# Optimization experiments

Measured on AMD Instinct MI355X. Metric: run time of the kernel, lower is better.

The kernel has to match this reference:

```python
import jax, jax.numpy as jnp
import numpy as np

IN_FEATURES = 4096
OUT_FEATURES = 11008
BATCH, SEQ = 4, 2048


def setup_inputs() -> dict:
    key = jax.random.key(0)
    k_x, k_w, k_b = jax.random.split(key, 3)
    x = jax.random.normal(k_x, (BATCH, SEQ, IN_FEATURES), dtype=jnp.float32)
    # int8-valued quantized weight (stored int32 for portability; values in [-127,127])
    weight_int8 = jax.random.randint(k_w, (OUT_FEATURES, IN_FEATURES), -127, 128, dtype=jnp.int32)
    # per-tensor symmetric quantization scale (max|w|/127 in original; any positive scalar)
    scale = jnp.float32(0.01)
    bias = jax.random.normal(k_b, (OUT_FEATURES,), dtype=jnp.float32) * 0.02
    return {"x": x, "weight_int8": weight_int8, "scale": scale, "bias": bias}


def reference(x, weight_int8, scale, bias):
    # Codec is lossless: decompress() yields the int8 tensor exactly, then
    # dequantizes: w = int8.astype(float) * scale; forward is F.linear(x, w, bias).
    w = weight_int8.astype(jnp.float32) * scale  # [out, in]
    # x: [b, s, in] @ w.T -> [b, s, out]
    return jnp.einsum("bsi,oi->bso", x, w) + bias
```

## Files before the change

kernel.cpp:

```cpp
#include <hip/hip_runtime.h>
#include <stdint.h>


#define M_DIM 8192
#define N_DIM 11008
#define K_DIM 4096

#define BM 256
#define BN 256
#define BK 32
#define NT (K_DIM / BK)
#define NBN (N_DIM / BN)
#define NBM (M_DIM / BM)
#define GRID (NBM * NBN)

typedef short bf16x8 __attribute__((ext_vector_type(8)));
typedef float f32x4 __attribute__((ext_vector_type(4)));
typedef float fvec4 __attribute__((ext_vector_type(4)));
typedef int   ivec4 __attribute__((ext_vector_type(4)));
typedef unsigned short usvec4 __attribute__((ext_vector_type(4)));

__device__ __forceinline__ unsigned short f2bf(float f) {
    union { float f; uint32_t u; } c; c.f = f;
    uint32_t u = c.u;
    return (unsigned short)((u + 0x7FFFu + ((u >> 16) & 1u)) >> 16);
}

__global__ __launch_bounds__(256) void cvt_fused_kernel(
    const float* __restrict__ x, const int* __restrict__ w,
    unsigned short* __restrict__ xo, unsigned short* __restrict__ wo)
{
    const int NX4 = M_DIM * K_DIM / 4;
    const int NW4 = N_DIM * K_DIM / 4;
    const int stride = gridDim.x * blockDim.x;
    const int t0 = blockIdx.x * blockDim.x + threadIdx.x;
    for (int i = t0; i < NX4; i += stride) {
        fvec4 v = __builtin_nontemporal_load(&((const fvec4*)x)[i]);
        usvec4 r;
        r.x = f2bf(v.x); r.y = f2bf(v.y); r.z = f2bf(v.z); r.w = f2bf(v.w);
        ((usvec4*)xo)[i] = r;
    }
    for (int i = t0; i < NW4; i += stride) {
        ivec4 v = __builtin_nontemporal_load(&((const ivec4*)w)[i]);
        usvec4 r;
        r.x = f2bf((float)v.x); r.y = f2bf((float)v.y);
        r.z = f2bf((float)v.z); r.w = f2bf((float)v.w);
        ((usvec4*)wo)[i] = r;
    }
}

__device__ __forceinline__ void async16(const void* g, void* l) {
    __builtin_amdgcn_global_load_lds((__attribute__((address_space(1))) void*)g,
                                     (__attribute__((address_space(3))) void*)l,
                                     16, 0, 0);
}


__global__ __launch_bounds__(512, 2) void gemm_bf16_kernel(
    const unsigned short* __restrict__ A,
    const unsigned short* __restrict__ B,
    const float* __restrict__ scale_p,
    const float* __restrict__ bias,
    float* __restrict__ out)
{
    __shared__ __attribute__((aligned(16))) char lds[131072];

    const int t    = threadIdx.x;
    const int lane = t & 63;
    const int w    = t >> 6;
    const int wm   = w >> 2;
    const int wn   = w & 3;
    const int quad = lane >> 4;
    const int l16  = lane & 15;

    const int bid = blockIdx.x;
    const int swz = (bid & 7) * (GRID / 8) + (bid >> 3);
    const int bm = swz / NBN;
    const int bn = swz % NBN;

    f32x4 acc[8][4];
#pragma unroll
    for (int i = 0; i < 8; i++)
#pragma unroll
        for (int j = 0; j < 4; j++)
            acc[i][j] = (f32x4){0.f, 0.f, 0.f, 0.f};

    const int rowh = t >> 2;
    const int slot = t & 3;
    const int csw  = ((slot ^ ((rowh >> 1) & 3)) << 4);
    const char* aS0 = (const char*)(A + (size_t)(bm * BM + rowh) * K_DIM) + csw;
    const char* bS0 = (const char*)(B + (size_t)(bn * BN + rowh) * K_DIM) + csw;
    const char* aS1 = aS0 + (size_t)128 * K_DIM * 2;
    const char* bS1 = bS0 + (size_t)128 * K_DIM * 2;
    char* aD = lds + t * 16;
    char* bD = lds + 65536 + t * 16;

#define STAGE(buf, kt) do { \
        const size_t kb_ = (size_t)(kt) * (BK * 2); \
        async16(aS0 + kb_, aD + ((buf) << 14)); \
        async16(aS1 + kb_, aD + ((buf) << 14) + 8192); \
        async16(bS0 + kb_, bD + ((buf) << 14)); \
        async16(bS1 + kb_, bD + ((buf) << 14) + 8192); \
    } while (0)

    const int coff = ((quad ^ ((l16 >> 1) & 3)) << 4);
    const int aoff = (wm * 128 + l16) * (BK * 2) + coff;
    const int boff = 65536 + (wn * 64 + l16) * (BK * 2) + coff;

    bf16x8 fa[8], fb[4], ga[8], gb[4];

    STAGE(0, 0); STAGE(1, 1); STAGE(2, 2);
    asm volatile("s_waitcnt vmcnt(8)" ::: "memory");
    __builtin_amdgcn_s_barrier();
    asm volatile("" ::: "memory");
#pragma unroll
    for (int j = 0; j < 4; j++) fb[j] = *(const bf16x8*)(lds + boff + j * 1024);
#pragma unroll
    for (int i = 0; i < 8; i++) fa[i] = *(const bf16x8*)(lds + aoff + i * 1024);

    auto body = [&](int kt, bf16x8 (&ca)[8], bf16x8 (&cb)[4],
                    bf16x8 (&na)[8], bf16x8 (&nb)[4]) __attribute__((always_inline)) {
        STAGE((kt + 3) & 3, (kt + 3) & (NT - 1));
        asm volatile("s_waitcnt vmcnt(8)" ::: "memory");
        __builtin_amdgcn_s_barrier();
        asm volatile("" ::: "memory");

        const char* Abn = lds + (((kt + 1) & 3) << 14) + aoff;
        const char* Bbn = lds + (((kt + 1) & 3) << 14) + boff;
#pragma unroll
        for (int j = 0; j < 4; j++) nb[j] = *(const bf16x8*)(Bbn + j * 1024);
#pragma unroll
        for (int i = 0; i < 8; i++) na[i] = *(const bf16x8*)(Abn + i * 1024);

        __builtin_amdgcn_s_setprio(1);
#pragma unroll
        for (int i = 0; i < 8; i++)
#pragma unroll
            for (int j = 0; j < 4; j++)
                acc[i][j] = __builtin_amdgcn_mfma_f32_16x16x32_bf16(
                    ca[i], cb[j], acc[i][j], 0, 0, 0);
        __builtin_amdgcn_s_setprio(0);
    };

    for (int kt = 0; kt < NT; kt += 2) {
        body(kt,     fa, fb, ga, gb);
        body(kt + 1, ga, gb, fa, fb);
    }
#undef STAGE

    const float scale = *scale_p;
    const int gcol = bn * BN + wn * 64 + l16;
    float bvals[4];
#pragma unroll
    for (int j = 0; j < 4; j++) bvals[j] = bias[gcol + j * 16];

#pragma unroll
    for (int i = 0; i < 8; i++) {
        const int grow0 = bm * BM + wm * 128 + i * 16 + quad * 4;
#pragma unroll
        for (int r = 0; r < 4; r++) {
            float* orow = out + (size_t)(grow0 + r) * N_DIM + gcol;
#pragma unroll
            for (int j = 0; j < 4; j++)
                orow[j * 16] = acc[i][j][r] * scale + bvals[j];
        }
    }
}

__global__ __launch_bounds__(256) void naive_kernel(
    const float* __restrict__ x, const int* __restrict__ w8,
    const float* __restrict__ scale_p, const float* __restrict__ bias,
    float* __restrict__ out)
{
    size_t idx = (size_t)blockIdx.x * 256 + threadIdx.x;
    if (idx >= (size_t)M_DIM * N_DIM) return;
    int n = (int)(idx % N_DIM);
    size_t m = idx / N_DIM;
    const float* xr = x + m * K_DIM;
    const int* wr = w8 + (size_t)n * K_DIM;
    float acc = 0.f;
    for (int k = 0; k < K_DIM; k++) acc += xr[k] * (float)wr[k];
    out[idx] = acc * (*scale_p) + bias[n];
}

extern "C" void kernel_launch(void* const* d_in, const int* in_sizes, int n_in,
                              void* d_out, int out_size, void* d_ws, size_t ws_size,
                              hipStream_t stream) {
    const float* x     = (const float*)d_in[0];
    const int*   w8    = (const int*)d_in[1];
    const float* scale = (const float*)d_in[2];
    const float* bias  = (const float*)d_in[3];
    float* out = (float*)d_out;

    const size_t a_bytes = (size_t)M_DIM * K_DIM * 2;
    const size_t b_bytes = (size_t)N_DIM * K_DIM * 2;

    if (ws_size >= a_bytes + b_bytes) {
        unsigned short* a_bf = (unsigned short*)d_ws;
        unsigned short* b_bf = (unsigned short*)((char*)d_ws + a_bytes);
        cvt_fused_kernel<<<2048, 256, 0, stream>>>(x, w8, a_bf, b_bf);
        gemm_bf16_kernel<<<GRID, 512, 0, stream>>>(a_bf, b_bf, scale, bias, out);
    } else {
        size_t total = (size_t)M_DIM * N_DIM;
        naive_kernel<<<(unsigned)((total + 255) / 256), 256, 0, stream>>>(
            x, w8, scale, bias, out);
    }
}
```

Baseline: 1.182 ms.

## Make bf16 GEMM persistent with cross-tile prefetch and nontemporal stores

Converts the GEMM into a persistent kernel with 256 blocks. Each block walks a strided set of tiles within its XCD chunk and prefetches the next tile's first K stages while finishing the current one. The barrier now comes before issuing the next async stage, with a tighter vmcnt wait. Output stores use nontemporal hints, and the conversion kernel launches more blocks. This aims to remove per-tile prologue bubbles and launch tail costs. In exchange, the wave tail becomes coarse (5 vs 6 tiles per block) and the code is more complex.

```diff
diff --git a/kernel.cpp b/kernel.cpp
--- a/kernel.cpp
+++ b/kernel.cpp
@@ -13,6 +13,8 @@
 #define NBN (N_DIM / BN)
 #define NBM (M_DIM / BM)
 #define GRID (NBM * NBN)
+#define CHUNK (GRID / 8)
+#define RS ((size_t)128 * K_DIM * 2)
 
 typedef short bf16x8 __attribute__((ext_vector_type(8)));
 typedef float f32x4 __attribute__((ext_vector_type(4)));
@@ -56,7 +58,31 @@
 }
 
 
-__global__ __launch_bounds__(512, 2) void gemm_bf16_kernel(
+#define BODY(kt, ca, cb, na, nb, sa, sb, skt) do {                               \
+    asm volatile("s_waitcnt vmcnt(4)" ::: "memory");                             \
+    __builtin_amdgcn_s_barrier();                                                \
+    asm volatile("" ::: "memory");                                               \
+    { const int kb_ = (skt) * (BK * 2);                                          \
+      const int bo_ = (((kt) + 3) & 3) << 14;                                    \
+      async16((sa) + loff + kb_,      aD + bo_);                                 \
+      async16((sa) + loff + RS + kb_, aD + bo_ + 8192);                          \
+      async16((sb) + loff + kb_,      bD + bo_);                                 \
+      async16((sb) + loff + RS + kb_, bD + bo_ + 8192); }                        \
+    { const char* Abn_ = lds + ((((kt) + 1) & 3) << 14) + aoff;                  \
+      const char* Bbn_ = lds + ((((kt) + 1) & 3) << 14) + boff;                  \
+      _Pragma("unroll") for (int j_ = 0; j_ < 4; j_++)                           \
+          nb[j_] = *(const bf16x8*)(Bbn_ + j_ * 1024);                           \
+      _Pragma("unroll") for (int i_ = 0; i_ < 8; i_++)                           \
+          na[i_] = *(const bf16x8*)(Abn_ + i_ * 1024); }                         \
+    __builtin_amdgcn_s_setprio(1);                                               \
+    _Pragma("unroll") for (int i_ = 0; i_ < 8; i_++)                             \
+    _Pragma("unroll") for (int j_ = 0; j_ < 4; j_++)                             \
+        acc[i_][j_] = __builtin_amdgcn_mfma_f32_16x16x32_bf16(                   \
+            ca[i_], cb[j_], acc[i_][j_], 0, 0, 0);                               \
+    __builtin_amdgcn_s_setprio(0);                                               \
+} while (0)
+
+__global__ __launch_bounds__(512, 2) void gemm_persistent(
     const unsigned short* __restrict__ A,
     const unsigned short* __restrict__ B,
     const float* __restrict__ scale_p,
@@ -73,10 +99,9 @@
     const int quad = lane >> 4;
     const int l16  = lane & 15;
 
-    const int bid = blockIdx.x;
-    const int swz = (bid & 7) * (GRID / 8) + (bid >> 3);
-    const int bm = swz / NBN;
-    const int bn = swz % NBN;
+    const int cu  = blockIdx.x;
+    const int xcd = cu & 7;
+    const int cui = cu >> 3;
 
     f32x4 acc[8][4];
 #pragma unroll
@@ -88,28 +113,33 @@
     const int rowh = t >> 2;
     const int slot = t & 3;
     const int csw  = ((slot ^ ((rowh >> 1) & 3)) << 4);
-    const char* aS0 = (const char*)(A + (size_t)(bm * BM + rowh) * K_DIM) + csw;
-    const char* bS0 = (const char*)(B + (size_t)(bn * BN + rowh) * K_DIM) + csw;
-    const char* aS1 = aS0 + (size_t)128 * K_DIM * 2;
-    const char* bS1 = bS0 + (size_t)128 * K_DIM * 2;
+    const size_t loff = (size_t)rowh * K_DIM * 2 + csw;
     char* aD = lds + t * 16;
     char* bD = lds + 65536 + t * 16;
-
-#define STAGE(buf, kt) do { \
-        const size_t kb_ = (size_t)(kt) * (BK * 2); \
-        async16(aS0 + kb_, aD + ((buf) << 14)); \
-        async16(aS1 + kb_, aD + ((buf) << 14) + 8192); \
-        async16(bS0 + kb_, bD + ((buf) << 14)); \
-        async16(bS1 + kb_, bD + ((buf) << 14) + 8192); \
-    } while (0)
 
     const int coff = ((quad ^ ((l16 >> 1) & 3)) << 4);
     const int aoff = (wm * 128 + l16) * (BK * 2) + coff;
     const int boff = 65536 + (wn * 64 + l16) * (BK * 2) + coff;
 
+    const float scale = *scale_p;
+
     bf16x8 fa[8], fb[4], ga[8], gb[4];
 
-    STAGE(0, 0); STAGE(1, 1); STAGE(2, 2);
+    int idx  = cui;
+    int tile = xcd * CHUNK + idx;
+    int bm = tile / NBN, bn = tile - bm * NBN;
+    const char* aCb = (const char*)A + (size_t)bm * BM * K_DIM * 2;
+    const char* bCb = (const char*)B + (size_t)bn * BN * K_DIM * 2;
+
+#define STAGE0(ab, bb, buf, kt) do {                                             \
+        const int kb_ = (kt) * (BK * 2);                                         \
+        async16((ab) + loff + kb_,      aD + ((buf) << 14));                     \
+        async16((ab) + loff + RS + kb_, aD + ((buf) << 14) + 8192);              \
+        async16((bb) + loff + kb_,      bD + ((buf) << 14));                     \
+        async16((bb) + loff + RS + kb_, bD + ((buf) << 14) + 8192);              \
+    } while (0)
+
+    STAGE0(aCb, bCb, 0, 0); STAGE0(aCb, bCb, 1, 1); STAGE0(aCb, bCb, 2, 2);
     asm volatile("s_waitcnt vmcnt(8)" ::: "memory");
     __builtin_amdgcn_s_barrier();
     asm volatile("" ::: "memory");
@@ -118,53 +148,50 @@
 #pragma unroll
     for (int i = 0; i < 8; i++) fa[i] = *(const bf16x8*)(lds + aoff + i * 1024);
 
-    auto body = [&](int kt, bf16x8 (&ca)[8], bf16x8 (&cb)[4],
-                    bf16x8 (&na)[8], bf16x8 (&nb)[4]) __attribute__((always_inline)) {
-        STAGE((kt + 3) & 3, (kt + 3) & (NT - 1));
-        asm volatile("s_waitcnt vmcnt(8)" ::: "memory");
-        __builtin_amdgcn_s_barrier();
-        asm volatile("" ::: "memory");
-
-        const char* Abn = lds + (((kt + 1) & 3) << 14) + aoff;
-        const char* Bbn = lds + (((kt + 1) & 3) << 14) + boff;
-#pragma unroll
-        for (int j = 0; j < 4; j++) nb[j] = *(const bf16x8*)(Bbn + j * 1024);
-#pragma unroll
-        for (int i = 0; i < 8; i++) na[i] = *(const bf16x8*)(Abn + i * 1024);
-
-        __builtin_amdgcn_s_setprio(1);
-#pragma unroll
-        for (int i = 0; i < 8; i++)
-#pragma unroll
-            for (int j = 0; j < 4; j++)
-                acc[i][j] = __builtin_amdgcn_mfma_f32_16x16x32_bf16(
-                    ca[i], cb[j], acc[i][j], 0, 0, 0);
-        __builtin_amdgcn_s_setprio(0);
-    };
-
-    for (int kt = 0; kt < NT; kt += 2) {
-        body(kt,     fa, fb, ga, gb);
-        body(kt + 1, ga, gb, fa, fb);
-    }
-#undef STAGE
-
-    const float scale = *scale_p;
-    const int gcol = bn * BN + wn * 64 + l16;
-    float bvals[4];
-#pragma unroll
-    for (int j = 0; j < 4; j++) bvals[j] = bias[gcol + j * 16];
-
-#pragma unroll
-    for (int i = 0; i < 8; i++) {
-        const int grow0 = bm * BM + wm * 128 + i * 16 + quad * 4;
-#pragma unroll
-        for (int r = 0; r < 4; r++) {
-            float* orow = out + (size_t)(grow0 + r) * N_DIM + gcol;
-#pragma unroll
-            for (int j = 0; j < 4; j++)
-                orow[j * 16] = acc[i][j][r] * scale + bvals[j];
+    for (;;) {
+        const int nidx  = idx + 32;
+        const int ntile = (nidx < CHUNK) ? (xcd * CHUNK + nidx) : tile;
+        const int nbm = ntile / NBN, nbn = ntile - nbm * NBN;
+        const char* aNb = (const char*)A + (size_t)nbm * BM * K_DIM * 2;
+        const char* bNb = (const char*)B + (size_t)nbn * BN * K_DIM * 2;
+
+        for (int kt = 0; kt < 124; kt += 2) {
+            BODY(kt,     fa, fb, ga, gb, aCb, bCb, kt + 3);
+            BODY(kt + 1, ga, gb, fa, fb, aCb, bCb, kt + 4);
         }
-    }
+        BODY(124, fa, fb, ga, gb, aCb, bCb, 127);
+        BODY(125, ga, gb, fa, fb, aNb, bNb, 0);
+        BODY(126, fa, fb, ga, gb, aNb, bNb, 1);
+        BODY(127, ga, gb, fa, fb, aNb, bNb, 2);
+
+        {
+            const int gcol = bn * BN + wn * 64 + l16;
+            float bvals[4];
+#pragma unroll
+            for (int j = 0; j < 4; j++) bvals[j] = bias[gcol + j * 16];
+#pragma unroll
+            for (int i = 0; i < 8; i++) {
+                const int grow0 = bm * BM + wm * 128 + i * 16 + quad * 4;
+#pragma unroll
+                for (int r = 0; r < 4; r++) {
+                    float* orow = out + (size_t)(grow0 + r) * N_DIM + gcol;
+#pragma unroll
+                    for (int j = 0; j < 4; j++)
+                        __builtin_nontemporal_store(acc[i][j][r] * scale + bvals[j],
+                                                    orow + j * 16);
+                }
+            }
+#pragma unroll
+            for (int i = 0; i < 8; i++)
+#pragma unroll
+                for (int j = 0; j < 4; j++)
+                    acc[i][j] = (f32x4){0.f, 0.f, 0.f, 0.f};
+        }
+
+        if (nidx >= CHUNK) break;
+        idx = nidx; tile = ntile; bm = nbm; bn = nbn; aCb = aNb; bCb = bNb;
+    }
+#undef STAGE0
 }
 
 __global__ __launch_bounds__(256) void naive_kernel(
@@ -198,8 +225,8 @@
     if (ws_size >= a_bytes + b_bytes) {
         unsigned short* a_bf = (unsigned short*)d_ws;
         unsigned short* b_bf = (unsigned short*)((char*)d_ws + a_bytes);
-        cvt_fused_kernel<<<2048, 256, 0, stream>>>(x, w8, a_bf, b_bf);
-        gemm_bf16_kernel<<<GRID, 512, 0, stream>>>(a_bf, b_bf, scale, bias, out);
+        cvt_fused_kernel<<<4096, 256, 0, stream>>>(x, w8, a_bf, b_bf);
+        gemm_persistent<<<256, 512, 0, stream>>>(a_bf, b_bf, scale, bias, out);
     } else {
         size_t total = (size_t)M_DIM * N_DIM;
         naive_kernel<<<(unsigned)((total + 255) / 256), 256, 0, stream>>>(
```

Result: faster. 1.154 ms (-2.3%).
